# Performance work log

Hardware: AMD Instinct MI355X
Metric: run time of the kernel (lower is better)

The kernel has to match this reference:

```python
import jax, jax.numpy as jnp
import numpy as np

B, T, D, H, L = 2048, 512, 8, 20, 10  # batch, seq, input_dim, hidden_dim, num_layers


def setup_inputs() -> dict:
    key = jax.random.key(0)
    ks = jax.random.split(key, 10)
    s = 1.0 / np.sqrt(H)  # PyTorch nn.RNN / nn.Linear init bound
    u = lambda k, shape: jax.random.uniform(k, shape, jnp.float32, -s, s)
    return {
        "x": jax.random.normal(ks[0], (B, T, D), jnp.float32),
        "w_ih0": u(ks[1], (H, D)),        # layer-0 input weights
        "w_ih": u(ks[2], (L - 1, H, H)),  # layers 1..9 input weights
        "w_hh": u(ks[3], (L, H, H)),
        "b_ih": u(ks[4], (L, H)),
        "b_hh": u(ks[5], (L, H)),
        "fc_w": u(ks[6], (H, H)),
        "fc_b": u(ks[7], (H,)),
        "l2_w": u(ks[8], (1, H)),
        "l2_b": u(ks[9], (1,)),
    }


def reference(x, w_ih0, w_ih, w_hh, b_ih, b_hh, fc_w, fc_b, l2_w, l2_b):
    # 10-layer Elman RNN (tanh), batch_first, h0 = 0, eval mode (no dropout).
    Bn = x.shape[0]
    h0 = jnp.zeros((L, Bn, H), x.dtype)

    def step(h, x_t):  # h: [L, B, H], x_t: [B, D]
        hs = []
        inp = x_t
        for l in range(L):  # fixed small layer count -> unrolled
            Wi = w_ih0 if l == 0 else w_ih[l - 1]
            hl = jnp.tanh(inp @ Wi.T + b_ih[l] + h[l] @ w_hh[l].T + b_hh[l])
            hs.append(hl)
            inp = hl
        return jnp.stack(hs), hl  # carry, top-layer output

    _, out = jax.lax.scan(step, h0, jnp.swapaxes(x, 0, 1))  # out: [T, B, H]
    out = jnp.swapaxes(out, 0, 1)  # [B, T, H]
    # Time-independent MLP head (original loops over t; batched here, same math)
    y = jax.nn.relu(out @ fc_w.T + fc_b) @ l2_w.T + l2_b  # [B, T, 1]
    return y
```

## Files before the change

### kernel.cpp

```cpp
#include <hip/hip_runtime.h>

#if __has_builtin(__builtin_amdgcn_exp2f)
#define EXP2F(x) __builtin_amdgcn_exp2f(x)
#else
#define EXP2F(x) exp2f(x)
#endif
#if __has_builtin(__builtin_amdgcn_rcpf)
#define RCPF(x) __builtin_amdgcn_rcpf(x)
#else
#define RCPF(x) (1.0f / (x))
#endif

namespace {

constexpr int B_ = 2048, T_ = 512, D_ = 8, H_ = 20, L_ = 10;
constexpr int NG    = 16;
constexpr int PADK  = 40;
constexpr int NW    = 11;
constexpr int NTHR  = NW * 64;
constexpr int DEPTH = 4;
constexpr int SLOT_STRIDE  = L_ * NG * PADK;
constexpr int LAYER_STRIDE = NG * PADK;

typedef float f32x4 __attribute__((ext_vector_type(4)));
typedef short s16x8 __attribute__((ext_vector_type(8)));

#define LD4(p) (*reinterpret_cast<const f32x4*>(p))

__device__ __forceinline__ unsigned short f2bf(float f) {
    unsigned u = __builtin_bit_cast(unsigned, f);
    return (unsigned short)((u + 0x7FFFu + ((u >> 16) & 1u)) >> 16);
}
__device__ __forceinline__ float bf2f(unsigned short b) {
    return __builtin_bit_cast(float, (unsigned)b << 16);
}
__device__ __forceinline__ unsigned cvt_pk_bf16(float s0, float s1) {
    unsigned r;
    asm("v_cvt_pk_bf16_f32 %0, %1, %2" : "=v"(r) : "v"(s0), "v"(s1));
    return r;
}

__device__ __forceinline__ f32x4 mfma_bf16(s16x8 a, s16x8 b, f32x4 c) {
    return __builtin_amdgcn_mfma_f32_16x16x32_bf16(a, b, c, 0, 0, 0);
}

__device__ __forceinline__ float tanh_fast(float x) {
    float e = EXP2F(x * 2.8853900817779268f);
    return fmaf(-2.0f, RCPF(1.0f + e), 1.0f);
}

__device__ __forceinline__ void wait_ge(int* p, int v) {
    while (__hip_atomic_load(p, __ATOMIC_ACQUIRE,
                             __HIP_MEMORY_SCOPE_WORKGROUP) < v) {}
    __builtin_amdgcn_sched_barrier(0);
}

__global__ __launch_bounds__(NTHR) void rnn_async(
    const float* __restrict__ x,
    const float* __restrict__ w_ih0,
    const float* __restrict__ w_ih,
    const float* __restrict__ w_hh,
    const float* __restrict__ b_ih,
    const float* __restrict__ b_hh,
    const float* __restrict__ fc_w,
    const float* __restrict__ fc_b,
    const float* __restrict__ l2_w,
    const float* __restrict__ l2_b,
    float* __restrict__ out)
{
    __shared__ __align__(16) unsigned short h_lds[DEPTH][L_][NG][PADK];
    __shared__ int prog[16];

    const int tid = threadIdx.x;
    const int w   = tid >> 6;
    const int l   = tid & 63;
    const int col = l & 15;
    const int g   = l >> 4;
    const int bg  = blockIdx.x * NG;

    {
        uint4* p4 = reinterpret_cast<uint4*>(&h_lds[0][0][0][0]);
        const int n4 = DEPTH * L_ * NG * PADK / 8;
        for (int i = tid; i < n4; i += NTHR) p4[i] = make_uint4(0, 0, 0, 0);
        if (tid < 16) prog[tid] = 0;
    }

    s16x8 a0_hi = {0,0,0,0,0,0,0,0}, a0_lo = a0_hi, a1_hi = a0_hi, a1_lo = a0_hi;
    s16x8 h0_hi = a0_hi, h0_lo = a0_hi, h1_hi = a0_hi, h1_lo = a0_hi;
    f32x4 bias0 = {0.f, 0.f, 0.f, 0.f}, bias1 = bias0;
    f32x4 l2v0 = bias0, l2v1 = bias0;
    float l2bv = 0.f;
    const bool mt1ok = col < (H_ - 16);

    if (w < L_) {
        const int layer = w;
        #pragma unroll
        for (int e = 0; e < 8; ++e) {
            const int k = g * 8 + e;
            float wv0 = 0.f, wv1 = 0.f;
            if (layer == 0) {
                if (k < 16) {
                    wv0 = w_ih0[col * D_ + (k & 7)];
                    if (mt1ok) wv1 = w_ih0[(16 + col) * D_ + (k & 7)];
                }
            } else if (k < H_) {
                wv0 = w_ih[((layer - 1) * H_ + col) * H_ + k];
                if (mt1ok) wv1 = w_ih[((layer - 1) * H_ + 16 + col) * H_ + k];
            }
            unsigned short b0 = f2bf(wv0), b1 = f2bf(wv1);
            a0_hi[e] = (short)b0; a0_lo[e] = (short)f2bf(wv0 - bf2f(b0));
            a1_hi[e] = (short)b1; a1_lo[e] = (short)f2bf(wv1 - bf2f(b1));
            float uv0 = 0.f, uv1 = 0.f;
            if (k < H_) {
                uv0 = w_hh[(layer * H_ + col) * H_ + k];
                if (mt1ok) uv1 = w_hh[(layer * H_ + 16 + col) * H_ + k];
            }
            unsigned short c0 = f2bf(uv0), c1 = f2bf(uv1);
            h0_hi[e] = (short)c0; h0_lo[e] = (short)f2bf(uv0 - bf2f(c0));
            h1_hi[e] = (short)c1; h1_lo[e] = (short)f2bf(uv1 - bf2f(c1));
        }
        #pragma unroll
        for (int r = 0; r < 4; ++r) {
            const int row = g * 4 + r;
            bias0[r] = b_ih[layer * H_ + row] + b_hh[layer * H_ + row];
            bias1[r] = (g == 0) ? (b_ih[layer * H_ + 16 + r] +
                                   b_hh[layer * H_ + 16 + r]) : 0.f;
        }
    } else {
        #pragma unroll
        for (int e = 0; e < 8; ++e) {
            const int k = g * 8 + e;
            float f0 = 0.f, f1 = 0.f;
            if (k < H_) {
                f0 = fc_w[col * H_ + k];
                if (mt1ok) f1 = fc_w[(16 + col) * H_ + k];
            }
            unsigned short b0 = f2bf(f0), b1 = f2bf(f1);
            a0_hi[e] = (short)b0; a0_lo[e] = (short)f2bf(f0 - bf2f(b0));
            a1_hi[e] = (short)b1; a1_lo[e] = (short)f2bf(f1 - bf2f(b1));
        }
        #pragma unroll
        for (int r = 0; r < 4; ++r) {
            bias0[r] = fc_b[g * 4 + r];
            bias1[r] = (g == 0) ? fc_b[16 + r] : 0.f;
            l2v0[r]  = l2_w[g * 4 + r];
            l2v1[r]  = (g == 0) ? l2_w[16 + r] : 0.f;
        }
        l2bv = l2_b[0];
    }

    f32x4 xc0 = {0.f,0.f,0.f,0.f}, xc1 = xc0, xn0 = xc0, xn1 = xc0;
    if (w == 0 && g < 2) {
        const float* xp = x + (size_t)(bg + col) * T_ * D_;
        xc0 = LD4(xp);      xc1 = LD4(xp + 4);
        xn0 = LD4(xp + D_); xn1 = LD4(xp + D_ + 4);
    }

    __syncthreads();

    unsigned short* const hb = &h_lds[0][0][0][0];
    const f32x4 z4 = {0.f, 0.f, 0.f, 0.f};

    if (w < L_) {
        const int rdB1 = w * LAYER_STRIDE + col * PADK + g * 8;
        const int rdB0 = (w ? (w - 1) * LAYER_STRIDE : 0) + col * PADK + g * 8;
        const int wr0  = w * LAYER_STRIDE + col * PADK + g * 4;
        const int wr1  = w * LAYER_STRIDE + col * PADK + 16;
        for (int t = 0; t < T_; ++t) {
            const int s_cur = (t & 3) * SLOT_STRIDE;
            const int s_prv = ((t + 3) & 3) * SLOT_STRIDE;
            s16x8 B1 = *reinterpret_cast<const s16x8*>(hb + s_prv + rdB1);
            if (t >= DEPTH) wait_ge(&prog[w + 1], t - (DEPTH - 1));
            s16x8 B0;
            if (w == 0) {
                s16x8 xf = {0,0,0,0,0,0,0,0};
                if (g < 2) {
                    #pragma unroll
                    for (int e = 0; e < 8; ++e) {
                        float f = (e < 4) ? xc0[e] : xc1[e - 4];
                        unsigned short hbit = f2bf(f);
                        xf[e] = (short)((g == 0) ? hbit : f2bf(f - bf2f(hbit)));
                    }
                    xc0 = xn0; xc1 = xn1;
                    if (t + 2 < T_) {
                        const float* xp = x + ((size_t)(bg + col) * T_ + t + 2) * D_;
                        xn0 = LD4(xp); xn1 = LD4(xp + 4);
                    }
                }
                B0 = xf;
            } else {
                wait_ge(&prog[w - 1], t + 1);
                B0 = *reinterpret_cast<const s16x8*>(hb + s_cur + rdB0);
            }
            f32x4 A  = mfma_bf16(h0_hi, B1, bias0);
            f32x4 Ab = mfma_bf16(h0_lo, B1, z4);
            f32x4 C  = mfma_bf16(h1_hi, B1, bias1);
            f32x4 Cb = mfma_bf16(h1_lo, B1, z4);
            A  = mfma_bf16(a0_hi, B0, A);
            Ab = mfma_bf16(a0_lo, B0, Ab);
            C  = mfma_bf16(a1_hi, B0, C);
            Cb = mfma_bf16(a1_lo, B0, Cb);
            f32x4 acc0 = A + Ab, acc1 = C + Cb;
            uint2 pw;
            pw.x = cvt_pk_bf16(tanh_fast(acc0[0]), tanh_fast(acc0[1]));
            pw.y = cvt_pk_bf16(tanh_fast(acc0[2]), tanh_fast(acc0[3]));
            *reinterpret_cast<uint2*>(hb + s_cur + wr0) = pw;
            if (g == 0) {
                uint2 qw;
                qw.x = cvt_pk_bf16(tanh_fast(acc1[0]), tanh_fast(acc1[1]));
                qw.y = cvt_pk_bf16(tanh_fast(acc1[2]), tanh_fast(acc1[3]));
                *reinterpret_cast<uint2*>(hb + s_cur + wr1) = qw;
            }
            if (l == 0)
                __hip_atomic_store(&prog[w], t + 1, __ATOMIC_RELEASE,
                                   __HIP_MEMORY_SCOPE_WORKGROUP);
        }
    } else {
        const int rdH = (L_ - 1) * LAYER_STRIDE + col * PADK + g * 8;
        for (int t = 0; t < T_; ++t) {
            wait_ge(&prog[L_ - 1], t + 1);
            s16x8 Bh = *reinterpret_cast<const s16x8*>(
                hb + (t & 3) * SLOT_STRIDE + rdH);
            f32x4 z0 = mfma_bf16(a0_hi, Bh, bias0);
            z0 = mfma_bf16(a0_lo, Bh, z0);
            f32x4 z1 = mfma_bf16(a1_hi, Bh, bias1);
            z1 = mfma_bf16(a1_lo, Bh, z1);
            float part = 0.f;
            #pragma unroll
            for (int r = 0; r < 4; ++r) {
                part = fmaf(l2v0[r], fmaxf(z0[r], 0.f), part);
                part = fmaf(l2v1[r], fmaxf(z1[r], 0.f), part);
            }
            part += __shfl_xor(part, 16);
            part += __shfl_xor(part, 32);
            if (l < NG) out[(size_t)(bg + l) * T_ + t] = part + l2bv;
            if (l == 0)
                __hip_atomic_store(&prog[L_], t + 1, __ATOMIC_RELEASE,
                                   __HIP_MEMORY_SCOPE_WORKGROUP);
        }
    }
}

}

extern "C" void kernel_launch(void* const* d_in, const int* in_sizes, int n_in,
                              void* d_out, int out_size, void* d_ws, size_t ws_size,
                              hipStream_t stream) {
    const float* x     = (const float*)d_in[0];
    const float* w_ih0 = (const float*)d_in[1];
    const float* w_ih  = (const float*)d_in[2];
    const float* w_hh  = (const float*)d_in[3];
    const float* b_ih  = (const float*)d_in[4];
    const float* b_hh  = (const float*)d_in[5];
    const float* fc_w  = (const float*)d_in[6];
    const float* fc_b  = (const float*)d_in[7];
    const float* l2_w  = (const float*)d_in[8];
    const float* l2_b  = (const float*)d_in[9];
    float* out = (float*)d_out;

    const int grid = B_ / NG;
    hipLaunchKernelGGL(rnn_async, dim3(grid), dim3(NTHR), 0, stream,
                       x, w_ih0, w_ih, w_hh, b_ih, b_hh, fc_w, fc_b,
                       l2_w, l2_b, out);
}
```

Baseline: 357.3 us.

## Defer downstream wait to store, lighter publish, deeper x prefetch, split head MFMA chains

Moves the wait on the downstream layer's progress from before the MFMAs to just before the LDS store, so compute proceeds while the consumer catches up. Replaces the release atomic store with an explicit lgkmcnt wait plus a relaxed store. The x prefetch depth grows from two to three steps. The head's dependent MFMA chains are split into independent ones that are summed. The relaxed publish relies on the explicit waitcnt for ordering, so correctness depends on LDS write visibility within the workgroup.

```diff
diff --git a/kernel.cpp b/kernel.cpp
--- a/kernel.cpp
+++ b/kernel.cpp
@@ -53,6 +53,11 @@
     while (__hip_atomic_load(p, __ATOMIC_ACQUIRE,
                              __HIP_MEMORY_SCOPE_WORKGROUP) < v) {}
     __builtin_amdgcn_sched_barrier(0);
+}
+
+__device__ __forceinline__ void publish(int* p, int v) {
+    asm volatile("s_waitcnt lgkmcnt(0)" ::: "memory");
+    __hip_atomic_store(p, v, __ATOMIC_RELAXED, __HIP_MEMORY_SCOPE_WORKGROUP);
 }
 
 __global__ __launch_bounds__(NTHR) void rnn_async(
@@ -149,11 +154,13 @@
         l2bv = l2_b[0];
     }
 
-    f32x4 xc0 = {0.f,0.f,0.f,0.f}, xc1 = xc0, xn0 = xc0, xn1 = xc0;
+    f32x4 xq0a = {0.f,0.f,0.f,0.f}, xq0b = xq0a;
+    f32x4 xq1a = xq0a, xq1b = xq0a, xq2a = xq0a, xq2b = xq0a;
     if (w == 0 && g < 2) {
         const float* xp = x + (size_t)(bg + col) * T_ * D_;
-        xc0 = LD4(xp);      xc1 = LD4(xp + 4);
-        xn0 = LD4(xp + D_); xn1 = LD4(xp + D_ + 4);
+        xq0a = LD4(xp);          xq0b = LD4(xp + 4);
+        xq1a = LD4(xp + D_);     xq1b = LD4(xp + D_ + 4);
+        xq2a = LD4(xp + 2 * D_); xq2b = LD4(xp + 2 * D_ + 4);
     }
 
     __syncthreads();
@@ -170,21 +177,21 @@
             const int s_cur = (t & 3) * SLOT_STRIDE;
             const int s_prv = ((t + 3) & 3) * SLOT_STRIDE;
             s16x8 B1 = *reinterpret_cast<const s16x8*>(hb + s_prv + rdB1);
-            if (t >= DEPTH) wait_ge(&prog[w + 1], t - (DEPTH - 1));
             s16x8 B0;
             if (w == 0) {
                 s16x8 xf = {0,0,0,0,0,0,0,0};
                 if (g < 2) {
                     #pragma unroll
                     for (int e = 0; e < 8; ++e) {
-                        float f = (e < 4) ? xc0[e] : xc1[e - 4];
+                        float f = (e < 4) ? xq0a[e] : xq0b[e - 4];
                         unsigned short hbit = f2bf(f);
                         xf[e] = (short)((g == 0) ? hbit : f2bf(f - bf2f(hbit)));
                     }
-                    xc0 = xn0; xc1 = xn1;
-                    if (t + 2 < T_) {
-                        const float* xp = x + ((size_t)(bg + col) * T_ + t + 2) * D_;
-                        xn0 = LD4(xp); xn1 = LD4(xp + 4);
+                    xq0a = xq1a; xq0b = xq1b;
+                    xq1a = xq2a; xq1b = xq2b;
+                    if (t + 3 < T_) {
+                        const float* xp = x + ((size_t)(bg + col) * T_ + t + 3) * D_;
+                        xq2a = LD4(xp); xq2b = LD4(xp + 4);
                     }
                 }
                 B0 = xf;
@@ -204,16 +211,16 @@
             uint2 pw;
             pw.x = cvt_pk_bf16(tanh_fast(acc0[0]), tanh_fast(acc0[1]));
             pw.y = cvt_pk_bf16(tanh_fast(acc0[2]), tanh_fast(acc0[3]));
-            *reinterpret_cast<uint2*>(hb + s_cur + wr0) = pw;
+            uint2 qw = make_uint2(0u, 0u);
             if (g == 0) {
-                uint2 qw;
                 qw.x = cvt_pk_bf16(tanh_fast(acc1[0]), tanh_fast(acc1[1]));
                 qw.y = cvt_pk_bf16(tanh_fast(acc1[2]), tanh_fast(acc1[3]));
+            }
+            if (t >= DEPTH) wait_ge(&prog[w + 1], t - (DEPTH - 1));
+            *reinterpret_cast<uint2*>(hb + s_cur + wr0) = pw;
+            if (g == 0)
                 *reinterpret_cast<uint2*>(hb + s_cur + wr1) = qw;
-            }
-            if (l == 0)
-                __hip_atomic_store(&prog[w], t + 1, __ATOMIC_RELEASE,
-                                   __HIP_MEMORY_SCOPE_WORKGROUP);
+            if (l == 0) publish(&prog[w], t + 1);
         }
     } else {
         const int rdH = (L_ - 1) * LAYER_STRIDE + col * PADK + g * 8;
@@ -221,10 +228,11 @@
             wait_ge(&prog[L_ - 1], t + 1);
             s16x8 Bh = *reinterpret_cast<const s16x8*>(
                 hb + (t & 3) * SLOT_STRIDE + rdH);
-            f32x4 z0 = mfma_bf16(a0_hi, Bh, bias0);
-            z0 = mfma_bf16(a0_lo, Bh, z0);
-            f32x4 z1 = mfma_bf16(a1_hi, Bh, bias1);
-            z1 = mfma_bf16(a1_lo, Bh, z1);
+            f32x4 z0  = mfma_bf16(a0_hi, Bh, bias0);
+            f32x4 z0b = mfma_bf16(a0_lo, Bh, z4);
+            f32x4 z1  = mfma_bf16(a1_hi, Bh, bias1);
+            f32x4 z1b = mfma_bf16(a1_lo, Bh, z4);
+            z0 += z0b; z1 += z1b;
             float part = 0.f;
             #pragma unroll
             for (int r = 0; r < 4; ++r) {
@@ -234,9 +242,7 @@
             part += __shfl_xor(part, 16);
             part += __shfl_xor(part, 32);
             if (l < NG) out[(size_t)(bg + l) * T_ + t] = part + l2bv;
-            if (l == 0)
-                __hip_atomic_store(&prog[L_], t + 1, __ATOMIC_RELEASE,
-                                   __HIP_MEMORY_SCOPE_WORKGROUP);
+            if (l == 0) publish(&prog[L_], t + 1);
         }
     }
 }
```

New measurement: 361.1 us. No clear change (+1.1%).
